# Optimization experiments

Measured on AMD Instinct MI355X. Metric: run time of the kernel, lower is better.

## Reference

```python
import jax, jax.numpy as jnp
import numpy as np


def setup_inputs() -> dict:
    key = jax.random.key(0)
    k1, k2, k3, k4 = jax.random.split(key, 4)
    B, D, N, M = 4, 256, 4096, 4096
    return {
        "src": jax.random.normal(k1, (B, 3, N), dtype=jnp.float32),
        "tgt": jax.random.normal(k2, (B, 3, M), dtype=jnp.float32),
        "src_emb": jax.random.normal(k3, (B, D, N), dtype=jnp.float32),
        "tgt_emb": jax.random.normal(k4, (B, D, M), dtype=jnp.float32),
    }


def reference(src, tgt, src_emb, tgt_emb):
    # pairwise_distance[b,n,m] = -||src_emb[:,n] - tgt_emb[:,m]||^2
    # decomposed as -xx + 2*inner - yy (inner below is -2*dot, as in torch code)
    inner = -2.0 * jnp.einsum("bdn,bdm->bnm", src_emb, tgt_emb)       # [B,N,M]
    xx = jnp.sum(src_emb ** 2, axis=1)[:, :, None]                     # [B,N,1]
    yy = jnp.sum(tgt_emb ** 2, axis=1)[:, None, :]                     # [B,1,M]
    pairwise_distance = -xx - inner - yy                               # [B,N,M]
    scores = jax.nn.softmax(pairwise_distance, axis=2)                 # softmax over tgt points
    # src_corr[b,c,n] = sum_m tgt[b,c,m] * scores[b,n,m]
    src_corr = jnp.einsum("bcm,bnm->bcn", tgt, scores)                 # [B,3,N]
    return src_corr
```

## Files before the change

kernel.cpp:

```cpp
#include <hip/hip_runtime.h>

#define NBATCH 4
#define DDIM   256
#define NN     4096
#define MM     4096
#define NCHUNK 8
#define MCHUNK 512
#define MTILE  32
#define LOG2E  1.44269504088896340736f

using half8   = __attribute__((ext_vector_type(8))) _Float16;
using floatx4 = __attribute__((ext_vector_type(4))) float;

__global__ __launch_bounds__(256) void k_prep(const float* __restrict__ src_emb,
                                              const float* __restrict__ tgt_emb,
                                              const float* __restrict__ tgt,
                                              _Float16* __restrict__ Qh,
                                              _Float16* __restrict__ Kh,
                                              float* __restrict__ yyS,
                                              float4* __restrict__ Vt) {
    __shared__ float psum[4][64];
    int i = blockIdx.x;
    int xcd = i & 7, j = i >> 3;
    int b = xcd >> 1, nhalf = xcd & 1;
    int tensor = j & 1, sub = j >> 1;
    int n0 = nhalf * 2048 + sub * 64;
    const float* in = tensor ? tgt_emb : src_emb;
    _Float16* outp  = tensor ? Kh : Qh;
    const float scale = tensor ? 1.0f : 2.0f * LOG2E;
    int t = threadIdx.x, w = t >> 6, ln = t & 63;
    const float* ib = in + (size_t)b * DDIM * NN + n0 + ln;
    _Float16* op = outp + (size_t)(b * NN + n0 + ln) * DDIM;
    float ss = 0.f;
#pragma unroll
    for (int itr = 0; itr < 8; itr++) {
        int dg = w + itr * 4;
        half8 h;
#pragma unroll
        for (int k = 0; k < 8; k++) {
            float f = ib[(size_t)(dg * 8 + k) * NN];
            ss = fmaf(f, f, ss);
            h[k] = (_Float16)(f * scale);
        }
        *(half8*)(op + dg * 8) = h;
    }
    if (tensor) psum[w][ln] = ss;
    __syncthreads();
    if (tensor) {
        if (t < 64) {
            float s = psum[0][t] + psum[1][t] + psum[2][t] + psum[3][t];
            yyS[b * MM + n0 + t] = s * (-LOG2E);
        } else if (t < 128) {
            int m = n0 + (t - 64);
            const float* tp = tgt + (size_t)b * 3 * MM + m;
            Vt[(size_t)b * MM + m] = make_float4(tp[0], tp[MM], tp[2 * MM], 1.0f);
        }
    }
}

__global__ __launch_bounds__(256) void k_flash(const _Float16* __restrict__ Qh,
                                               const _Float16* __restrict__ Kh,
                                               const float* __restrict__ yyS,
                                               const float4* __restrict__ Vt,
                                               float4* __restrict__ Opart,
                                               float* __restrict__ Mpart) {
    __shared__ __align__(16) _Float16 Kt[2][MTILE * DDIM];
    __shared__ floatx4 vtt[MCHUNK];
    __shared__ floatx4 yyt[MCHUNK / 4];

    int i = blockIdx.x, t = threadIdx.x;
    int xcd = i & 7, j = i >> 3;
    int b = xcd >> 1, nhalf = xcd & 1;
    int chunk = j & 7, ntile = nhalf * 8 + (j >> 3);

    int wave = t >> 6, lane = t & 63, quad = lane >> 4, l15 = lane & 15;
    int n0 = ntile * 256 + wave * 64;
    int m0 = chunk * MCHUNK;

    const _Float16* kp = Kh + (size_t)b * MM * DDIM;
    int dg = lane & 31, rh = lane >> 5;
    auto stage = [&](int mt) {
        const _Float16* gb = kp + (size_t)(m0 + mt * MTILE) * DDIM;
        _Float16* lb = &Kt[mt & 1][0];
#pragma unroll
        for (int it = 0; it < 4; it++) {
            int row = wave * 8 + it * 2 + rh;
            __builtin_amdgcn_global_load_lds(
                (const __attribute__((address_space(1))) uint32_t*)(const void*)
                    (gb + (size_t)row * DDIM + dg * 8),
                (__attribute__((address_space(3))) uint32_t*)(void*)
                    (lb + (wave * 8 + it * 2) * DDIM),
                16, 0, 0);
        }
    };

    stage(0);

    {
        const float4* vb = Vt + (size_t)b * MM + m0;
        for (int r = t; r < MCHUNK; r += 256) {
            float4 g = vb[r];
            vtt[r] = (floatx4){g.x, g.y, g.z, g.w};
        }
        const floatx4* yb = (const floatx4*)(yyS + (size_t)b * MM + m0);
        if (t < MCHUNK / 4) yyt[t] = yb[t];
    }

    const _Float16* qp = Qh + (size_t)b * NN * DDIM;
    half8 qf[4][8];
#pragma unroll
    for (int nb = 0; nb < 4; nb++) {
        int n = n0 + nb * 16 + l15;
#pragma unroll
        for (int ds = 0; ds < 8; ds++)
            qf[nb][ds] = *(const half8*)(qp + (size_t)n * DDIM + (ds * 4 + quad) * 8);
    }

    const floatx4 z4 = {0.f, 0.f, 0.f, 0.f};
    floatx4 o[4] = {z4, z4, z4, z4};
    float mr[4];
#pragma unroll
    for (int nb = 0; nb < 4; nb++) mr[nb] = -__builtin_inff();

    for (int mt = 0; mt < MCHUNK / MTILE; mt++) {
        __syncthreads();
        if (mt + 1 < MCHUNK / MTILE) stage(mt + 1);

        const _Float16* Kb = &Kt[mt & 1][0];
        floatx4 acc[4][2];
#pragma unroll
        for (int nb = 0; nb < 4; nb++) { acc[nb][0] = z4; acc[nb][1] = z4; }
#pragma unroll
        for (int ds = 0; ds < 8; ds++) {
            half8 a0 = *(const half8*)(Kb + (size_t)l15 * DDIM + (ds * 4 + quad) * 8);
            half8 a1 = *(const half8*)(Kb + (size_t)(16 + l15) * DDIM + (ds * 4 + quad) * 8);
#pragma unroll
            for (int nb = 0; nb < 4; nb++) {
                acc[nb][0] = __builtin_amdgcn_mfma_f32_16x16x32_f16(a0, qf[nb][ds], acc[nb][0], 0, 0, 0);
                acc[nb][1] = __builtin_amdgcn_mfma_f32_16x16x32_f16(a1, qf[nb][ds], acc[nb][1], 0, 0, 0);
            }
        }

        floatx4 yv0 = yyt[mt * 8 + quad];
        floatx4 yv1 = yyt[mt * 8 + 4 + quad];
#pragma unroll
        for (int nb = 0; nb < 4; nb++) {
            acc[nb][0] = acc[nb][0] + yv0;
            acc[nb][1] = acc[nb][1] + yv1;
            floatx4 mx = __builtin_elementwise_max(acc[nb][0], acc[nb][1]);
            float tm = fmaxf(fmaxf(mx[0], mx[1]), fmaxf(mx[2], mx[3]));
            float mn = fmaxf(mr[nb], tm);
            float al = __builtin_amdgcn_exp2f(mr[nb] - mn);
            mr[nb] = mn;
            o[nb] = o[nb] * al;
            floatx4 mnv = {mn, mn, mn, mn};
            acc[nb][0] = acc[nb][0] - mnv;
            acc[nb][1] = acc[nb][1] - mnv;
        }
#pragma unroll
        for (int mb = 0; mb < 2; mb++) {
            floatx4 vr[4];
#pragma unroll
            for (int r = 0; r < 4; r++) vr[r] = vtt[mt * 32 + mb * 16 + quad * 4 + r];
#pragma unroll
            for (int nb = 0; nb < 4; nb++)
#pragma unroll
                for (int r = 0; r < 4; r++) {
                    float p = __builtin_amdgcn_exp2f(acc[nb][mb][r]);
                    o[nb] = o[nb] + p * vr[r];
                }
        }
    }

#pragma unroll
    for (int nb = 0; nb < 4; nb++) {
        float mq = mr[nb];
        float ma = fmaxf(mq, __shfl_xor(mq, 16, 64));
        ma = fmaxf(ma, __shfl_xor(ma, 32, 64));
        float wgt = __builtin_amdgcn_exp2f(mq - ma);
        floatx4 ow = o[nb] * wgt;
#pragma unroll
        for (int c = 0; c < 4; c++) {
            float v = ow[c];
            v += __shfl_xor(v, 16, 64);
            v += __shfl_xor(v, 32, 64);
            ow[c] = v;
        }
        if (quad == 0) {
            int n = n0 + nb * 16 + l15;
            size_t idx = (size_t)(chunk * NBATCH + b) * NN + n;
            Opart[idx] = make_float4(ow[0], ow[1], ow[2], ow[3]);
            Mpart[idx] = ma;
        }
    }
}

__global__ __launch_bounds__(128) void k_combine(const float4* __restrict__ Opart,
                                                 const float* __restrict__ Mpart,
                                                 float* __restrict__ out) {
    int idx = blockIdx.x * 128 + threadIdx.x;
    int b = idx >> 12, n = idx & (NN - 1);
    float mstar = -__builtin_inff();
#pragma unroll
    for (int j = 0; j < NCHUNK; j++)
        mstar = fmaxf(mstar, Mpart[(size_t)(j * NBATCH + b) * NN + n]);
    float o0 = 0.f, o1 = 0.f, o2 = 0.f, l = 0.f;
#pragma unroll
    for (int j = 0; j < NCHUNK; j++) {
        size_t id = (size_t)(j * NBATCH + b) * NN + n;
        float w = __builtin_amdgcn_exp2f(Mpart[id] - mstar);
        float4 P = Opart[id];
        o0 = fmaf(w, P.x, o0); o1 = fmaf(w, P.y, o1);
        o2 = fmaf(w, P.z, o2); l  = fmaf(w, P.w, l);
    }
    out[(size_t)(b * 3 + 0) * NN + n] = o0 / l;
    out[(size_t)(b * 3 + 1) * NN + n] = o1 / l;
    out[(size_t)(b * 3 + 2) * NN + n] = o2 / l;
}

extern "C" void kernel_launch(void* const* d_in, const int* in_sizes, int n_in,
                              void* d_out, int out_size, void* d_ws, size_t ws_size,
                              hipStream_t stream) {
    const float* tgt     = (const float*)d_in[1];
    const float* src_emb = (const float*)d_in[2];
    const float* tgt_emb = (const float*)d_in[3];
    float* out = (float*)d_out;

    char* ws = (char*)d_ws;
    _Float16* Qh  = (_Float16*)(ws);
    _Float16* Kh  = (_Float16*)(ws + 8388608);
    float*    yyS = (float*)   (ws + 16777216);
    float4*   Vt  = (float4*)  (ws + 16842752);
    float4*   Op  = (float4*)  (ws + 17104896);
    float*    Mp  = (float*)   (ws + 19202048);

    hipLaunchKernelGGL(k_prep,    dim3(512), dim3(256), 0, stream,
                       src_emb, tgt_emb, tgt, Qh, Kh, yyS, Vt);
    hipLaunchKernelGGL(k_flash,   dim3(512), dim3(256), 0, stream, Qh, Kh, yyS, Vt, Op, Mp);
    hipLaunchKernelGGL(k_combine, dim3(128), dim3(128), 0, stream, Op, Mp, out);
}
```

Measured before the change: 155.5 us.

## Double K tile to 64 rows with padded LDS layout and per-subblock online softmax

Doubles the staged K tile from 32 to 64 rows, so each chunk needs half as many barriers and stage steps. K rows are stored in LDS as padded row pairs (1040-byte stride) to reduce bank conflicts on the fragment reads. The softmax rescale now runs per 16-row subblock, reading all 8 K fragments of a subblock before its MFMAs. Occupancy is hinted at 2 blocks per CU. The cost is about twice the LDS per block and more frequent max/rescale exp2 work.

New measurement: 133.4 us. 14.2% less time.

```diff
diff --git a/kernel.cpp b/kernel.cpp
--- a/kernel.cpp
+++ b/kernel.cpp
@@ -6,7 +6,9 @@
 #define MM     4096
 #define NCHUNK 8
 #define MCHUNK 512
-#define MTILE  32
+#define MTILE  64
+#define PAIRB  1040
+#define SUBB   (32 * PAIRB)
 #define LOG2E  1.44269504088896340736f
 
 using half8   = __attribute__((ext_vector_type(8))) _Float16;
@@ -58,13 +60,13 @@
     }
 }
 
-__global__ __launch_bounds__(256) void k_flash(const _Float16* __restrict__ Qh,
-                                               const _Float16* __restrict__ Kh,
-                                               const float* __restrict__ yyS,
-                                               const float4* __restrict__ Vt,
-                                               float4* __restrict__ Opart,
-                                               float* __restrict__ Mpart) {
-    __shared__ __align__(16) _Float16 Kt[2][MTILE * DDIM];
+__global__ __launch_bounds__(256, 2) void k_flash(const _Float16* __restrict__ Qh,
+                                                  const _Float16* __restrict__ Kh,
+                                                  const float* __restrict__ yyS,
+                                                  const float4* __restrict__ Vt,
+                                                  float4* __restrict__ Opart,
+                                                  float* __restrict__ Mpart) {
+    __shared__ __align__(16) char Kt[2 * SUBB];
     __shared__ floatx4 vtt[MCHUNK];
     __shared__ floatx4 yyt[MCHUNK / 4];
 
@@ -81,15 +83,15 @@
     int dg = lane & 31, rh = lane >> 5;
     auto stage = [&](int mt) {
         const _Float16* gb = kp + (size_t)(m0 + mt * MTILE) * DDIM;
-        _Float16* lb = &Kt[mt & 1][0];
-#pragma unroll
-        for (int it = 0; it < 4; it++) {
-            int row = wave * 8 + it * 2 + rh;
+        char* lb = &Kt[(mt & 1) * SUBB];
+#pragma unroll
+        for (int it = 0; it < 8; it++) {
+            int pr = wave * 8 + it;
             __builtin_amdgcn_global_load_lds(
                 (const __attribute__((address_space(1))) uint32_t*)(const void*)
-                    (gb + (size_t)row * DDIM + dg * 8),
+                    (gb + (size_t)(pr * 2 + rh) * DDIM + dg * 8),
                 (__attribute__((address_space(3))) uint32_t*)(void*)
-                    (lb + (wave * 8 + it * 2) * DDIM),
+                    (lb + pr * PAIRB),
                 16, 0, 0);
         }
     };
@@ -126,49 +128,41 @@
         __syncthreads();
         if (mt + 1 < MCHUNK / MTILE) stage(mt + 1);
 
-        const _Float16* Kb = &Kt[mt & 1][0];
-        floatx4 acc[4][2];
-#pragma unroll
-        for (int nb = 0; nb < 4; nb++) { acc[nb][0] = z4; acc[nb][1] = z4; }
-#pragma unroll
-        for (int ds = 0; ds < 8; ds++) {
-            half8 a0 = *(const half8*)(Kb + (size_t)l15 * DDIM + (ds * 4 + quad) * 8);
-            half8 a1 = *(const half8*)(Kb + (size_t)(16 + l15) * DDIM + (ds * 4 + quad) * 8);
+        const char* Kb = &Kt[(mt & 1) * SUBB];
+#pragma unroll
+        for (int mb = 0; mb < 4; mb++) {
+            half8 a[8];
+            {
+                int rho = mb * 16 + l15;
+                const char* rb = Kb + (rho >> 1) * PAIRB + (rho & 1) * 512 + quad * 16;
+#pragma unroll
+                for (int ds = 0; ds < 8; ds++) a[ds] = *(const half8*)(rb + ds * 64);
+            }
+            floatx4 acc[4] = {z4, z4, z4, z4};
+#pragma unroll
+            for (int ds = 0; ds < 8; ds++)
+#pragma unroll
+                for (int nb = 0; nb < 4; nb++)
+                    acc[nb] = __builtin_amdgcn_mfma_f32_16x16x32_f16(a[ds], qf[nb][ds], acc[nb], 0, 0, 0);
+
+            floatx4 yv = yyt[mt * 16 + mb * 4 + quad];
+            floatx4 vr[4];
+#pragma unroll
+            for (int r = 0; r < 4; r++) vr[r] = vtt[mt * MTILE + mb * 16 + quad * 4 + r];
 #pragma unroll
             for (int nb = 0; nb < 4; nb++) {
-                acc[nb][0] = __builtin_amdgcn_mfma_f32_16x16x32_f16(a0, qf[nb][ds], acc[nb][0], 0, 0, 0);
-                acc[nb][1] = __builtin_amdgcn_mfma_f32_16x16x32_f16(a1, qf[nb][ds], acc[nb][1], 0, 0, 0);
-            }
-        }
-
-        floatx4 yv0 = yyt[mt * 8 + quad];
-        floatx4 yv1 = yyt[mt * 8 + 4 + quad];
-#pragma unroll
-        for (int nb = 0; nb < 4; nb++) {
-            acc[nb][0] = acc[nb][0] + yv0;
-            acc[nb][1] = acc[nb][1] + yv1;
-            floatx4 mx = __builtin_elementwise_max(acc[nb][0], acc[nb][1]);
-            float tm = fmaxf(fmaxf(mx[0], mx[1]), fmaxf(mx[2], mx[3]));
-            float mn = fmaxf(mr[nb], tm);
-            float al = __builtin_amdgcn_exp2f(mr[nb] - mn);
-            mr[nb] = mn;
-            o[nb] = o[nb] * al;
-            floatx4 mnv = {mn, mn, mn, mn};
-            acc[nb][0] = acc[nb][0] - mnv;
-            acc[nb][1] = acc[nb][1] - mnv;
-        }
-#pragma unroll
-        for (int mb = 0; mb < 2; mb++) {
-            floatx4 vr[4];
-#pragma unroll
-            for (int r = 0; r < 4; r++) vr[r] = vtt[mt * 32 + mb * 16 + quad * 4 + r];
-#pragma unroll
-            for (int nb = 0; nb < 4; nb++)
+                acc[nb] = acc[nb] + yv;
+                float tm = fmaxf(fmaxf(acc[nb][0], acc[nb][1]), fmaxf(acc[nb][2], acc[nb][3]));
+                float mn = fmaxf(mr[nb], tm);
+                float al = __builtin_amdgcn_exp2f(mr[nb] - mn);
+                mr[nb] = mn;
+                o[nb] = o[nb] * al;
 #pragma unroll
                 for (int r = 0; r < 4; r++) {
-                    float p = __builtin_amdgcn_exp2f(acc[nb][mb][r]);
+                    float p = __builtin_amdgcn_exp2f(acc[nb][r] - mn);
                     o[nb] = o[nb] + p * vr[r];
                 }
+            }
         }
     }
 
```
